# Kernel optimization log

Hardware: AMD Instinct MI355X
Metric: run time of the kernel (lower is better)

## Reference

```python
import jax, jax.numpy as jnp
import numpy as np

UNITS = 80
LATENT = 128
IN_DIM = 256
BATCH = 8192
SIZE = 256


def _lstm_zero_state_step(x, K, b):
    """One Keras LSTM step from zero (h0, c0). activation=relu, recurrent_activation=sigmoid.
    With h0=0 the recurrent kernel contributes nothing; with c0=0 the forget gate is inert.
    Keras gate order in kernel/bias: i, f, c, o."""
    z = x @ K + b                       # (B, 4*UNITS)
    zi, zf, zc, zo = jnp.split(z, 4, axis=-1)
    c = jax.nn.sigmoid(zi) * jax.nn.relu(zc)   # i * act(c_tilde)
    return jax.nn.sigmoid(zo) * jax.nn.relu(c) # o * act(c)


def setup_inputs() -> dict:
    key = jax.random.key(0)
    ks = jax.random.split(key, 9)
    s = 0.05
    return {
        "x": jax.random.normal(ks[0], (BATCH, IN_DIM), jnp.float32),
        "size": SIZE,
        "W_lat": jax.random.normal(ks[1], (IN_DIM, LATENT), jnp.float32) * s,
        "b_lat": jax.random.normal(ks[2], (LATENT,), jnp.float32) * s,
        "K_fw": jax.random.normal(ks[3], (LATENT, 4 * UNITS), jnp.float32) * s,
        "b_fw": jax.random.normal(ks[4], (4 * UNITS,), jnp.float32) * s,
        "K_bw": jax.random.normal(ks[5], (LATENT, 4 * UNITS), jnp.float32) * s,
        "b_bw": jax.random.normal(ks[6], (4 * UNITS,), jnp.float32) * s,
        "K_1": jax.random.normal(ks[7], (2 * UNITS, 4 * UNITS), jnp.float32) * s,
        "b_1": jax.random.normal(ks[8], (4 * UNITS,), jnp.float32) * s,
    }


def reference(x, size, W_lat, b_lat, K_fw, b_fw, K_bw, b_bw, K_1, b_1):
    # Dense latent projection
    lat = x @ W_lat + b_lat                      # (B, 128)

    def decode_step(inp):                        # inp: (B, 128)
        # Bidirectional over a length-1 sequence: fw and bw both see the same
        # single timestep; merge mode is concat([forward, backward]).
        h_fw = _lstm_zero_state_step(inp, K_fw, b_fw)
        h_bw = _lstm_zero_state_step(inp, K_bw, b_bw)
        h = jnp.concatenate([h_fw, h_bw], axis=-1)   # (B, 160)
        return _lstm_zero_state_step(h, K_1, b_1)    # (B, 80)

    # The original Python loop feeds the latent vector only on iteration 0;
    # every later iteration feeds tf.ones(x_shape), and all Keras layers are
    # stateless (fresh zero state each call), so steps 1..size-1 are identical.
    y0 = decode_step(lat)                         # (B, 80)
    yc = decode_step(jnp.ones_like(lat))          # (B, 80)
    B = x.shape[0]
    rest = jnp.broadcast_to(yc[:, None, :], (B, size - 1, UNITS))
    return jnp.concatenate([y0[:, None, :], rest], axis=1)  # (B, size, 80)
```

## Files before the change

kernel.cpp:

```cpp
#include <hip/hip_runtime.h>
#include <math.h>

#define UNITS 80
#define LATENT 128
#define IN_DIM 256
#define BATCH 8192
#define SEQ 256
#define G 320
#define H2 160

#define TPB 640
#define RPB 4
#define NBLK (BATCH / RPB)

typedef float f4 __attribute__((ext_vector_type(4)));

__device__ __forceinline__ float sigf(float v) {
    return 1.0f / (1.0f + __expf(-v));
}

__global__ __launch_bounds__(640)
void yc_kernel(const float* __restrict__ Kf, const float* __restrict__ bf,
               const float* __restrict__ Kb, const float* __restrict__ bb,
               const float* __restrict__ K1, const float* __restrict__ b1,
               float* __restrict__ yc) {
    __shared__ float z[2 * G];
    __shared__ float h[H2];
    const int t = threadIdx.x;

    {
        const float* K   = (t < G) ? Kf : Kb;
        const float* bia = (t < G) ? bf : bb;
        const int c = (t < G) ? t : t - G;
        float acc = bia[c];
#pragma unroll 8
        for (int l = 0; l < LATENT; ++l) acc += K[l * G + c];
        z[t] = acc;
    }
    __syncthreads();
    if (t < UNITS) {
        h[t] = sigf(z[240 + t]) * sigf(z[t]) * fmaxf(z[160 + t], 0.f);
    } else if (t >= G && t < G + UNITS) {
        const int u = t - G;
        h[UNITS + u] = sigf(z[G + 240 + u]) * sigf(z[G + u]) * fmaxf(z[G + 160 + u], 0.f);
    }
    __syncthreads();
    if (t < G) {
        float acc = b1[t];
#pragma unroll 8
        for (int l = 0; l < H2; ++l) acc = fmaf(h[l], K1[l * G + t], acc);
        z[t] = acc;
    }
    __syncthreads();
    if (t < UNITS) yc[t] = sigf(z[240 + t]) * sigf(z[t]) * fmaxf(z[160 + t], 0.f);
}

__global__ __launch_bounds__(TPB)
void main_kernel(const float* __restrict__ x,
                 const float* __restrict__ Wl, const float* __restrict__ bl,
                 const float* __restrict__ Kf, const float* __restrict__ bf,
                 const float* __restrict__ Kb, const float* __restrict__ bb,
                 const float* __restrict__ K1, const float* __restrict__ b1,
                 const float* __restrict__ yc,
                 float* __restrict__ out) {
    __shared__ float xs[RPB * IN_DIM];
    __shared__ float lat_s[RPB * LATENT];
    __shared__ float h_s[RPB * H2];
    __shared__ f4 yc4s[UNITS / 4];

    const int t = threadIdx.x;
    const int R0 = blockIdx.x * RPB;

    if (t < UNITS / 4) yc4s[t] = ((const f4*)yc)[t];
    {
        const f4* xg = (const f4*)(x + (size_t)R0 * IN_DIM);
        f4* xs4 = (f4*)xs;
        if (t < RPB * IN_DIM / 4) xs4[t] = xg[t];
    }
    __syncthreads();

    {
        const f4 yv = yc4s[t % (UNITS / 4)];
        f4* out4 = (f4*)out;
        const int per_row = (SEQ - 1) * UNITS / 4;
#pragma unroll
        for (int r = 0; r < RPB; ++r) {
            f4* rowp = out4 + (size_t)(R0 + r) * (SEQ * UNITS / 4) + (UNITS / 4);
#pragma unroll
            for (int k = 0; k < 8; ++k) {
                const int j = t + k * TPB;
                if (j < per_row) __builtin_nontemporal_store(yv, rowp + j);
            }
        }
    }

    if (t < 512) {
        const int row = t >> 7, col = t & 127;
        float acc = bl[col];
        const float* xr = xs + row * IN_DIM;
#pragma unroll 8
        for (int l = 0; l < IN_DIM; ++l) acc = fmaf(xr[l], Wl[l * LATENT + col], acc);
        lat_s[row * LATENT + col] = acc;
    }
    __syncthreads();

    {
        const int half = t / G;
        const int tt = t - half * G;
        const int row = tt / UNITS;
        const int u = tt - row * UNITS;
        const float* K   = half ? Kb : Kf;
        const float* bia = half ? bb : bf;
        float ai = 0.f, ac = 0.f, ao = 0.f;
        const float* lr = lat_s + row * LATENT;
#pragma unroll 4
        for (int k = 0; k < LATENT; ++k) {
            const float lv = lr[k];
            ai = fmaf(lv, K[k * G + u], ai);
            ac = fmaf(lv, K[k * G + 160 + u], ac);
            ao = fmaf(lv, K[k * G + 240 + u], ao);
        }
        h_s[row * H2 + half * UNITS + u] =
            sigf(ao + bia[240 + u]) * sigf(ai + bia[u]) * fmaxf(ac + bia[160 + u], 0.f);
    }
    __syncthreads();

    if (t < G) {
        const int row = t / UNITS;
        const int u = t - row * UNITS;
        float ai = 0.f, ac = 0.f, ao = 0.f;
        const float* hr = h_s + row * H2;
#pragma unroll 4
        for (int k = 0; k < H2; ++k) {
            const float hv = hr[k];
            ai = fmaf(hv, K1[k * G + u], ai);
            ac = fmaf(hv, K1[k * G + 160 + u], ac);
            ao = fmaf(hv, K1[k * G + 240 + u], ao);
        }
        const float y = sigf(ao + b1[240 + u]) * sigf(ai + b1[u]) * fmaxf(ac + b1[160 + u], 0.f);
        __builtin_nontemporal_store(y, out + (size_t)(R0 + row) * SEQ * UNITS + u);
    }
}

extern "C" void kernel_launch(void* const* d_in, const int* in_sizes, int n_in,
                              void* d_out, int out_size, void* d_ws, size_t ws_size,
                              hipStream_t stream) {
    const float* x   = (const float*)d_in[0];
    const float* Wl  = (const float*)d_in[2];
    const float* bl  = (const float*)d_in[3];
    const float* Kf  = (const float*)d_in[4];
    const float* bf  = (const float*)d_in[5];
    const float* Kb  = (const float*)d_in[6];
    const float* bb  = (const float*)d_in[7];
    const float* K1  = (const float*)d_in[8];
    const float* b1  = (const float*)d_in[9];
    float* out = (float*)d_out;
    float* yc  = (float*)d_ws;

    yc_kernel<<<1, 640, 0, stream>>>(Kf, bf, Kb, bb, K1, b1, yc);
    main_kernel<<<NBLK, TPB, 0, stream>>>(x, Wl, bl, Kf, bf, Kb, bb, K1, b1, yc, out);
}
```

Before: 201.5 us.

## Split compute and broadcast-write into separate kernels, fold yc into compute

Moves the constant-row computation into block 0 of a new compute kernel, which also processes 16 rows per block instead of 4 to reuse weight loads across more rows. The bulk broadcast write of the repeated output rows moves into a separate pure-store writer kernel that runs after the compute kernel. The aim is to separate the bandwidth-bound store stream from the compute phase and to amortise weight traffic. The cost is that the compute kernel now runs fewer blocks with loops per thread, and the two phases are serialised rather than interleaved.

```diff
diff --git a/kernel.cpp b/kernel.cpp
--- a/kernel.cpp
+++ b/kernel.cpp
@@ -8,10 +8,14 @@
 #define SEQ 256
 #define G 320
 #define H2 160
+#define ROW_F4 (SEQ * UNITS / 4)
+#define BODY_F4 ((SEQ - 1) * UNITS / 4)
 
 #define TPB 640
-#define RPB 4
-#define NBLK (BATCH / RPB)
+#define RPB_C 16
+#define NCB (BATCH / RPB_C)
+#define RPB_W 4
+#define NWB (BATCH / RPB_W)
 
 typedef float f4 __attribute__((ext_vector_type(4)));
 
@@ -19,96 +23,75 @@
     return 1.0f / (1.0f + __expf(-v));
 }
 
-__global__ __launch_bounds__(640)
-void yc_kernel(const float* __restrict__ Kf, const float* __restrict__ bf,
-               const float* __restrict__ Kb, const float* __restrict__ bb,
-               const float* __restrict__ K1, const float* __restrict__ b1,
-               float* __restrict__ yc) {
+__global__ __launch_bounds__(TPB)
+void compute_kernel(const float* __restrict__ x,
+                    const float* __restrict__ Wl, const float* __restrict__ bl,
+                    const float* __restrict__ Kf, const float* __restrict__ bf,
+                    const float* __restrict__ Kb, const float* __restrict__ bb,
+                    const float* __restrict__ Kw1, const float* __restrict__ b1,
+                    float* __restrict__ yc, float* __restrict__ out) {
+    __shared__ float xs[RPB_C * IN_DIM];
+    __shared__ float lat_s[RPB_C * LATENT];
+    __shared__ float h_s[RPB_C * H2];
     __shared__ float z[2 * G];
-    __shared__ float h[H2];
-    const int t = threadIdx.x;
-
-    {
-        const float* K   = (t < G) ? Kf : Kb;
-        const float* bia = (t < G) ? bf : bb;
-        const int c = (t < G) ? t : t - G;
-        float acc = bia[c];
-#pragma unroll 8
-        for (int l = 0; l < LATENT; ++l) acc += K[l * G + c];
-        z[t] = acc;
-    }
-    __syncthreads();
-    if (t < UNITS) {
-        h[t] = sigf(z[240 + t]) * sigf(z[t]) * fmaxf(z[160 + t], 0.f);
-    } else if (t >= G && t < G + UNITS) {
-        const int u = t - G;
-        h[UNITS + u] = sigf(z[G + 240 + u]) * sigf(z[G + u]) * fmaxf(z[G + 160 + u], 0.f);
-    }
-    __syncthreads();
-    if (t < G) {
-        float acc = b1[t];
-#pragma unroll 8
-        for (int l = 0; l < H2; ++l) acc = fmaf(h[l], K1[l * G + t], acc);
-        z[t] = acc;
-    }
-    __syncthreads();
-    if (t < UNITS) yc[t] = sigf(z[240 + t]) * sigf(z[t]) * fmaxf(z[160 + t], 0.f);
-}
-
-__global__ __launch_bounds__(TPB)
-void main_kernel(const float* __restrict__ x,
-                 const float* __restrict__ Wl, const float* __restrict__ bl,
-                 const float* __restrict__ Kf, const float* __restrict__ bf,
-                 const float* __restrict__ Kb, const float* __restrict__ bb,
-                 const float* __restrict__ K1, const float* __restrict__ b1,
-                 const float* __restrict__ yc,
-                 float* __restrict__ out) {
-    __shared__ float xs[RPB * IN_DIM];
-    __shared__ float lat_s[RPB * LATENT];
-    __shared__ float h_s[RPB * H2];
-    __shared__ f4 yc4s[UNITS / 4];
+    __shared__ float hh[H2];
 
     const int t = threadIdx.x;
-    const int R0 = blockIdx.x * RPB;
+    const int bid = blockIdx.x;
 
-    if (t < UNITS / 4) yc4s[t] = ((const f4*)yc)[t];
+    if (bid == 0) {
+        {
+            const float* K   = (t < G) ? Kf : Kb;
+            const float* bia = (t < G) ? bf : bb;
+            const int c = (t < G) ? t : t - G;
+            float acc = bia[c];
+#pragma unroll 8
+            for (int l = 0; l < LATENT; ++l) acc += K[l * G + c];
+            z[t] = acc;
+        }
+        __syncthreads();
+        if (t < UNITS) {
+            hh[t] = sigf(z[240 + t]) * sigf(z[t]) * fmaxf(z[160 + t], 0.f);
+        } else if (t >= G && t < G + UNITS) {
+            const int u = t - G;
+            hh[UNITS + u] = sigf(z[G + 240 + u]) * sigf(z[G + u]) * fmaxf(z[G + 160 + u], 0.f);
+        }
+        __syncthreads();
+        if (t < G) {
+            float acc = b1[t];
+#pragma unroll 8
+            for (int l = 0; l < H2; ++l) acc = fmaf(hh[l], Kw1[l * G + t], acc);
+            z[t] = acc;
+        }
+        __syncthreads();
+        if (t < UNITS) yc[t] = sigf(z[240 + t]) * sigf(z[t]) * fmaxf(z[160 + t], 0.f);
+        return;
+    }
+
+    const int R0 = (bid - 1) * RPB_C;
+
     {
         const f4* xg = (const f4*)(x + (size_t)R0 * IN_DIM);
         f4* xs4 = (f4*)xs;
-        if (t < RPB * IN_DIM / 4) xs4[t] = xg[t];
+        for (int i = t; i < RPB_C * IN_DIM / 4; i += TPB) xs4[i] = xg[i];
     }
     __syncthreads();
 
-    {
-        const f4 yv = yc4s[t % (UNITS / 4)];
-        f4* out4 = (f4*)out;
-        const int per_row = (SEQ - 1) * UNITS / 4;
-#pragma unroll
-        for (int r = 0; r < RPB; ++r) {
-            f4* rowp = out4 + (size_t)(R0 + r) * (SEQ * UNITS / 4) + (UNITS / 4);
-#pragma unroll
-            for (int k = 0; k < 8; ++k) {
-                const int j = t + k * TPB;
-                if (j < per_row) __builtin_nontemporal_store(yv, rowp + j);
-            }
-        }
-    }
-
-    if (t < 512) {
-        const int row = t >> 7, col = t & 127;
+    for (int i = t; i < RPB_C * LATENT; i += TPB) {
+        const int row = i >> 7, col = i & 127;
         float acc = bl[col];
         const float* xr = xs + row * IN_DIM;
 #pragma unroll 8
         for (int l = 0; l < IN_DIM; ++l) acc = fmaf(xr[l], Wl[l * LATENT + col], acc);
-        lat_s[row * LATENT + col] = acc;
+        lat_s[i] = acc;
     }
     __syncthreads();
 
-    {
-        const int half = t / G;
-        const int tt = t - half * G;
-        const int row = tt / UNITS;
-        const int u = tt - row * UNITS;
+    for (int i = t; i < 2 * RPB_C * UNITS; i += TPB) {
+        const int half = (i >= RPB_C * UNITS);
+        const int j = half ? i - RPB_C * UNITS : i;
+        const int row = j / UNITS;
+        const int u = j - row * UNITS;
         const float* K   = half ? Kb : Kf;
         const float* bia = half ? bb : bf;
         float ai = 0.f, ac = 0.f, ao = 0.f;
@@ -125,20 +108,40 @@
     }
     __syncthreads();
 
-    if (t < G) {
-        const int row = t / UNITS;
-        const int u = t - row * UNITS;
+    for (int i = t; i < RPB_C * UNITS; i += TPB) {
+        const int row = i / UNITS;
+        const int u = i - row * UNITS;
         float ai = 0.f, ac = 0.f, ao = 0.f;
         const float* hr = h_s + row * H2;
 #pragma unroll 4
         for (int k = 0; k < H2; ++k) {
             const float hv = hr[k];
-            ai = fmaf(hv, K1[k * G + u], ai);
-            ac = fmaf(hv, K1[k * G + 160 + u], ac);
-            ao = fmaf(hv, K1[k * G + 240 + u], ao);
+            ai = fmaf(hv, Kw1[k * G + u], ai);
+            ac = fmaf(hv, Kw1[k * G + 160 + u], ac);
+            ao = fmaf(hv, Kw1[k * G + 240 + u], ao);
         }
         const float y = sigf(ao + b1[240 + u]) * sigf(ai + b1[u]) * fmaxf(ac + b1[160 + u], 0.f);
         __builtin_nontemporal_store(y, out + (size_t)(R0 + row) * SEQ * UNITS + u);
+    }
+}
+
+__global__ __launch_bounds__(TPB)
+void writer_kernel(const float* __restrict__ yc, float* __restrict__ out) {
+    __shared__ f4 ycs[UNITS / 4];
+    const int t = threadIdx.x;
+    if (t < UNITS / 4) ycs[t] = ((const f4*)yc)[t];
+    __syncthreads();
+    const f4 yv = ycs[t % (UNITS / 4)];
+
+    f4* rowp = (f4*)out + (size_t)blockIdx.x * RPB_W * ROW_F4 + (UNITS / 4);
+#pragma unroll
+    for (int r = 0; r < RPB_W; ++r) {
+#pragma unroll
+        for (int k = 0; k < 8; ++k) {
+            const int j = t + k * TPB;
+            if (j < BODY_F4) __builtin_nontemporal_store(yv, rowp + j);
+        }
+        rowp += ROW_F4;
     }
 }
 
@@ -152,11 +155,11 @@
     const float* bf  = (const float*)d_in[5];
     const float* Kb  = (const float*)d_in[6];
     const float* bb  = (const float*)d_in[7];
-    const float* K1  = (const float*)d_in[8];
+    const float* Kw1 = (const float*)d_in[8];
     const float* b1  = (const float*)d_in[9];
     float* out = (float*)d_out;
     float* yc  = (float*)d_ws;
 
-    yc_kernel<<<1, 640, 0, stream>>>(Kf, bf, Kb, bb, K1, b1, yc);
-    main_kernel<<<NBLK, TPB, 0, stream>>>(x, Wl, bl, Kf, bf, Kb, bb, K1, b1, yc, out);
+    compute_kernel<<<NCB + 1, TPB, 0, stream>>>(x, Wl, bl, Kf, bf, Kb, bb, Kw1, b1, yc, out);
+    writer_kernel<<<NWB, TPB, 0, stream>>>(yc, out);
 }
```

Result: slower. 297.9 us (+47.8%).

## Split main kernel into dedicated broadcast-writer blocks and compute blocks

Applied to the files above, without the earlier changes.

Specializes the grid: the first 256 blocks only write the repeated yc broadcast (32 rows each), and 512 compute blocks each handle 16 rows of the latent projection and LSTM steps. Compute blocks get more reuse of the weight loads per block, and the store-bound broadcast is isolated into streaming writer blocks. Nontemporal stores are replaced with regular stores, and the final output stores are grouped after a sched barrier. This risks imbalance between writer and compute blocks and changes cache behaviour for the large output write.

```diff
diff --git a/kernel.cpp b/kernel.cpp
--- a/kernel.cpp
+++ b/kernel.cpp
@@ -8,10 +8,14 @@
 #define SEQ 256
 #define G 320
 #define H2 160
+#define ROW_F4 (SEQ * UNITS / 4)
+#define BODY_F4 ((SEQ - 1) * UNITS / 4)
 
-#define TPB 640
-#define RPB 4
-#define NBLK (BATCH / RPB)
+#define TPB 320
+#define NW 256
+#define ROWS_W (BATCH / NW)
+#define NC 512
+#define ROWS_C (BATCH / NC)
 
 typedef float f4 __attribute__((ext_vector_type(4)));
 
@@ -63,52 +67,55 @@
                  const float* __restrict__ K1, const float* __restrict__ b1,
                  const float* __restrict__ yc,
                  float* __restrict__ out) {
-    __shared__ float xs[RPB * IN_DIM];
-    __shared__ float lat_s[RPB * LATENT];
-    __shared__ float h_s[RPB * H2];
-    __shared__ f4 yc4s[UNITS / 4];
+    __shared__ float xs[ROWS_C * IN_DIM];
+    __shared__ float lat_s[ROWS_C * LATENT];
+    __shared__ float h_s[ROWS_C * H2];
 
     const int t = threadIdx.x;
-    const int R0 = blockIdx.x * RPB;
+    const int bid = blockIdx.x;
 
-    if (t < UNITS / 4) yc4s[t] = ((const f4*)yc)[t];
+    if (bid < NW) {
+        __shared__ f4 ycs[UNITS / 4];
+        if (t < UNITS / 4) ycs[t] = ((const f4*)yc)[t];
+        __syncthreads();
+        const f4 yv = ycs[t % (UNITS / 4)];
+
+        f4* rowp = (f4*)out + (size_t)bid * ROWS_W * ROW_F4 + (UNITS / 4);
+        for (int r = 0; r < ROWS_W; ++r) {
+#pragma unroll
+            for (int k = 0; k < 15; ++k)
+                rowp[t + k * TPB] = yv;
+            if (t < BODY_F4 - 15 * TPB)
+                rowp[t + 15 * TPB] = yv;
+            rowp += ROW_F4;
+        }
+        return;
+    }
+
+    const int R0 = (bid - NW) * ROWS_C;
+
     {
         const f4* xg = (const f4*)(x + (size_t)R0 * IN_DIM);
         f4* xs4 = (f4*)xs;
-        if (t < RPB * IN_DIM / 4) xs4[t] = xg[t];
+        for (int i = t; i < ROWS_C * IN_DIM / 4; i += TPB) xs4[i] = xg[i];
     }
     __syncthreads();
 
-    {
-        const f4 yv = yc4s[t % (UNITS / 4)];
-        f4* out4 = (f4*)out;
-        const int per_row = (SEQ - 1) * UNITS / 4;
-#pragma unroll
-        for (int r = 0; r < RPB; ++r) {
-            f4* rowp = out4 + (size_t)(R0 + r) * (SEQ * UNITS / 4) + (UNITS / 4);
-#pragma unroll
-            for (int k = 0; k < 8; ++k) {
-                const int j = t + k * TPB;
-                if (j < per_row) __builtin_nontemporal_store(yv, rowp + j);
-            }
-        }
-    }
-
-    if (t < 512) {
-        const int row = t >> 7, col = t & 127;
+    for (int i = t; i < ROWS_C * LATENT; i += TPB) {
+        const int row = i >> 7, col = i & 127;
         float acc = bl[col];
         const float* xr = xs + row * IN_DIM;
 #pragma unroll 8
         for (int l = 0; l < IN_DIM; ++l) acc = fmaf(xr[l], Wl[l * LATENT + col], acc);
-        lat_s[row * LATENT + col] = acc;
+        lat_s[i] = acc;
     }
     __syncthreads();
 
-    {
-        const int half = t / G;
-        const int tt = t - half * G;
-        const int row = tt / UNITS;
-        const int u = tt - row * UNITS;
+    for (int i = t; i < 2 * ROWS_C * UNITS; i += TPB) {
+        const int half = (i >= ROWS_C * UNITS);
+        const int j = half ? i - ROWS_C * UNITS : i;
+        const int row = j / UNITS;
+        const int u = j - row * UNITS;
         const float* K   = half ? Kb : Kf;
         const float* bia = half ? bb : bf;
         float ai = 0.f, ac = 0.f, ao = 0.f;
@@ -125,9 +132,12 @@
     }
     __syncthreads();
 
-    if (t < G) {
-        const int row = t / UNITS;
-        const int u = t - row * UNITS;
+    float yv0 = 0.f, yv1 = 0.f, yv2 = 0.f, yv3 = 0.f;
+#pragma unroll
+    for (int p = 0; p < 4; ++p) {
+        const int i = t + p * TPB;
+        const int row = i / UNITS;
+        const int u = i - row * UNITS;
         float ai = 0.f, ac = 0.f, ao = 0.f;
         const float* hr = h_s + row * H2;
 #pragma unroll 4
@@ -138,7 +148,18 @@
             ao = fmaf(hv, K1[k * G + 240 + u], ao);
         }
         const float y = sigf(ao + b1[240 + u]) * sigf(ai + b1[u]) * fmaxf(ac + b1[160 + u], 0.f);
-        __builtin_nontemporal_store(y, out + (size_t)(R0 + row) * SEQ * UNITS + u);
+        if (p == 0) yv0 = y; else if (p == 1) yv1 = y; else if (p == 2) yv2 = y; else yv3 = y;
+    }
+
+    __builtin_amdgcn_sched_barrier(0);
+
+#pragma unroll
+    for (int p = 0; p < 4; ++p) {
+        const int i = t + p * TPB;
+        const int row = i / UNITS;
+        const int u = i - row * UNITS;
+        const float y = (p == 0) ? yv0 : (p == 1) ? yv1 : (p == 2) ? yv2 : yv3;
+        out[(size_t)(R0 + row) * SEQ * UNITS + u] = y;
     }
 }
 
@@ -158,5 +179,5 @@
     float* yc  = (float*)d_ws;
 
     yc_kernel<<<1, 640, 0, stream>>>(Kf, bf, Kb, bb, K1, b1, yc);
-    main_kernel<<<NBLK, TPB, 0, stream>>>(x, Wl, bl, Kf, bf, Kb, bb, K1, b1, yc, out);
+    main_kernel<<<NW + NC, TPB, 0, stream>>>(x, Wl, bl, Kf, bf, Kb, bb, K1, b1, yc, out);
 }
```

Measured after the change: 362.0 us. 1.8x slower.

## Split block into compute waves per row and dedicated broadcast-store waves

Applied to the files above, without the earlier changes.

Each block now has 8 wavefronts. Four waves each compute one row's full LSTM chain, syncing only within the wave instead of with block-wide barriers. The other four waves immediately write most of the broadcast tail of their row and exit. The compute waves write their row's first output plus the remaining tail chunk. The aim is to overlap the dense matvec latency with the bulk output streaming and to remove the __syncthreads stalls. In exchange, each wave computes its row serially with more work per lane.

```diff
diff --git a/kernel.cpp b/kernel.cpp
--- a/kernel.cpp
+++ b/kernel.cpp
@@ -8,8 +8,12 @@
 #define SEQ 256
 #define G 320
 #define H2 160
+#define ROW_F (SEQ * UNITS)
+#define ROW_F4 (ROW_F / 4)
+#define BODY_F4 ((SEQ - 1) * UNITS / 4)
+#define SPLIT_F4 3840
 
-#define TPB 640
+#define TPB 512
 #define RPB 4
 #define NBLK (BATCH / RPB)
 
@@ -17,6 +21,11 @@
 
 __device__ __forceinline__ float sigf(float v) {
     return 1.0f / (1.0f + __expf(-v));
+}
+
+__device__ __forceinline__ void wave_sync() {
+    asm volatile("" ::: "memory");
+    __builtin_amdgcn_wave_barrier();
 }
 
 __global__ __launch_bounds__(640)
@@ -55,7 +64,7 @@
     if (t < UNITS) yc[t] = sigf(z[240 + t]) * sigf(z[t]) * fmaxf(z[160 + t], 0.f);
 }
 
-__global__ __launch_bounds__(TPB)
+__global__ __launch_bounds__(TPB, 4)
 void main_kernel(const float* __restrict__ x,
                  const float* __restrict__ Wl, const float* __restrict__ bl,
                  const float* __restrict__ Kf, const float* __restrict__ bf,
@@ -63,82 +72,104 @@
                  const float* __restrict__ K1, const float* __restrict__ b1,
                  const float* __restrict__ yc,
                  float* __restrict__ out) {
-    __shared__ float xs[RPB * IN_DIM];
-    __shared__ float lat_s[RPB * LATENT];
-    __shared__ float h_s[RPB * H2];
-    __shared__ f4 yc4s[UNITS / 4];
+    __shared__ float cws[4][544];
 
     const int t = threadIdx.x;
+    const int lane = t & 63;
+    const int w = t >> 6;
     const int R0 = blockIdx.x * RPB;
 
-    if (t < UNITS / 4) yc4s[t] = ((const f4*)yc)[t];
-    {
-        const f4* xg = (const f4*)(x + (size_t)R0 * IN_DIM);
-        f4* xs4 = (f4*)xs;
-        if (t < RPB * IN_DIM / 4) xs4[t] = xg[t];
+    f4 yvs[5];
+#pragma unroll
+    for (int p = 0; p < 5; ++p)
+        yvs[p] = ((const f4*)yc)[(lane + 4 * p) % (UNITS / 4)];
+
+    if (w >= 4) {
+        const int row = R0 + (w - 4);
+        f4* rowp = (f4*)out + (size_t)row * ROW_F4 + (UNITS / 4);
+        for (int g = 0; g < 12; ++g) {
+#pragma unroll
+            for (int p = 0; p < 5; ++p)
+                __builtin_nontemporal_store(yvs[p], rowp + (g * 5 + p) * 64 + lane);
+        }
+        return;
     }
-    __syncthreads();
+
+    const int row = R0 + w;
+    float* S = cws[w];
+    float* lat = S + 256;
+    float* h = S + 384;
+
+    ((f4*)S)[lane] = ((const f4*)(x + (size_t)row * IN_DIM))[lane];
+    wave_sync();
 
     {
-        const f4 yv = yc4s[t % (UNITS / 4)];
-        f4* out4 = (f4*)out;
-        const int per_row = (SEQ - 1) * UNITS / 4;
+        float a0 = bl[lane], a1 = bl[lane + 64];
+        for (int l = 0; l < IN_DIM; ++l) {
+            const float xv = S[l];
+            a0 = fmaf(xv, Wl[l * LATENT + lane], a0);
+            a1 = fmaf(xv, Wl[l * LATENT + lane + 64], a1);
+        }
+        lat[lane] = a0;
+        lat[lane + 64] = a1;
+    }
+    wave_sync();
+
 #pragma unroll
-        for (int r = 0; r < RPB; ++r) {
-            f4* rowp = out4 + (size_t)(R0 + r) * (SEQ * UNITS / 4) + (UNITS / 4);
+    for (int gidx = 0; gidx < 3; ++gidx) {
+        const int o = lane + gidx * 64;
+        if (o < H2) {
+            const int isbw = (o >= UNITS);
+            const int u = isbw ? o - UNITS : o;
+            const float* K   = isbw ? Kb : Kf;
+            const float* bia = isbw ? bb : bf;
+            float ai = bia[u], ac = bia[160 + u], ao = bia[240 + u];
+            for (int k = 0; k < LATENT; ++k) {
+                const float lv = lat[k];
+                ai = fmaf(lv, K[k * G + u], ai);
+                ac = fmaf(lv, K[k * G + 160 + u], ac);
+                ao = fmaf(lv, K[k * G + 240 + u], ao);
+            }
+            h[o] = sigf(ao) * sigf(ai) * fmaxf(ac, 0.f);
+        }
+    }
+    wave_sync();
+
+    {
+        const int u0 = lane;
+        const int u1 = (lane < 16) ? 64 + lane : 79;
+        float ai0 = b1[u0], ac0 = b1[160 + u0], ao0 = b1[240 + u0];
+        float ai1 = b1[u1], ac1 = b1[160 + u1], ao1 = b1[240 + u1];
+        for (int k = 0; k < H2; ++k) {
+            const float hv = h[k];
+            ai0 = fmaf(hv, K1[k * G + u0], ai0);
+            ac0 = fmaf(hv, K1[k * G + 160 + u0], ac0);
+            ao0 = fmaf(hv, K1[k * G + 240 + u0], ao0);
+            ai1 = fmaf(hv, K1[k * G + u1], ai1);
+            ac1 = fmaf(hv, K1[k * G + 160 + u1], ac1);
+            ao1 = fmaf(hv, K1[k * G + 240 + u1], ao1);
+        }
+        const float y0v = sigf(ao0) * sigf(ai0) * fmaxf(ac0, 0.f);
+        const float y1v = sigf(ao1) * sigf(ai1) * fmaxf(ac1, 0.f);
+        S[u0] = y0v;
+        if (lane < 16) S[u1] = y1v;
+    }
+    wave_sync();
+
+    if (lane < UNITS / 4) {
+        const f4 yq = ((const f4*)S)[lane];
+        __builtin_nontemporal_store(yq, (f4*)(out + (size_t)row * ROW_F) + lane);
+    }
+
+    {
+        f4* rowp = (f4*)out + (size_t)row * ROW_F4 + (UNITS / 4);
+        for (int g = 0; g < 4; ++g) {
 #pragma unroll
-            for (int k = 0; k < 8; ++k) {
-                const int j = t + k * TPB;
-                if (j < per_row) __builtin_nontemporal_store(yv, rowp + j);
+            for (int p = 0; p < 5; ++p) {
+                const int j = SPLIT_F4 + (g * 5 + p) * 64 + lane;
+                if (j < BODY_F4) __builtin_nontemporal_store(yvs[p], rowp + j);
             }
         }
-    }
-
-    if (t < 512) {
-        const int row = t >> 7, col = t & 127;
-        float acc = bl[col];
-        const float* xr = xs + row * IN_DIM;
-#pragma unroll 8
-        for (int l = 0; l < IN_DIM; ++l) acc = fmaf(xr[l], Wl[l * LATENT + col], acc);
-        lat_s[row * LATENT + col] = acc;
-    }
-    __syncthreads();
-
-    {
-        const int half = t / G;
-        const int tt = t - half * G;
-        const int row = tt / UNITS;
-        const int u = tt - row * UNITS;
-        const float* K   = half ? Kb : Kf;
-        const float* bia = half ? bb : bf;
-        float ai = 0.f, ac = 0.f, ao = 0.f;
-        const float* lr = lat_s + row * LATENT;
-#pragma unroll 4
-        for (int k = 0; k < LATENT; ++k) {
-            const float lv = lr[k];
-            ai = fmaf(lv, K[k * G + u], ai);
-            ac = fmaf(lv, K[k * G + 160 + u], ac);
-            ao = fmaf(lv, K[k * G + 240 + u], ao);
-        }
-        h_s[row * H2 + half * UNITS + u] =
-            sigf(ao + bia[240 + u]) * sigf(ai + bia[u]) * fmaxf(ac + bia[160 + u], 0.f);
-    }
-    __syncthreads();
-
-    if (t < G) {
-        const int row = t / UNITS;
-        const int u = t - row * UNITS;
-        float ai = 0.f, ac = 0.f, ao = 0.f;
-        const float* hr = h_s + row * H2;
-#pragma unroll 4
-        for (int k = 0; k < H2; ++k) {
-            const float hv = hr[k];
-            ai = fmaf(hv, K1[k * G + u], ai);
-            ac = fmaf(hv, K1[k * G + 160 + u], ac);
-            ao = fmaf(hv, K1[k * G + 240 + u], ao);
-        }
-        const float y = sigf(ao + b1[240 + u]) * sigf(ai + b1[u]) * fmaxf(ac + b1[160 + u], 0.f);
-        __builtin_nontemporal_store(y, out + (size_t)(R0 + row) * SEQ * UNITS + u);
     }
 }
 
```

Measured after the change: 217.0 us. +7.7%, slower.
